# Kernel optimization log

Measured on AMD Instinct MI355X. Metric: run time of the kernel, lower is better.

## Reference

```python
import jax, jax.numpy as jnp
import numpy as np

N = 10000        # total_num
BS = 100         # batch_size (BatchNorm is applied per micro-batch in train mode)
IN_CH = 3
D = 128          # out_channels
TOPK = 50
BN_EPS = 1e-5


def setup_inputs() -> dict:
    key = jax.random.key(0)
    k1, k2, k3, k4 = jax.random.split(key, 4)
    feat = 32 * 32 * IN_CH
    inputs = jax.random.normal(k1, (N, IN_CH, 32, 32), dtype=jnp.float32)
    # nn.Linear(32*32*in_channels, out_channels)
    W1 = jax.random.normal(k2, (D, feat), dtype=jnp.float32) / np.sqrt(feat)
    b1 = jnp.zeros((D,), jnp.float32)
    # BatchNorm1d(out_channels) affine params
    gamma = jnp.ones((D,), jnp.float32)
    beta = jnp.zeros((D,), jnp.float32)
    # nn.Linear(out_channels, 1) -> weight [1, D] stored as vector, scalar bias
    sw = jax.random.normal(k3, (D,), dtype=jnp.float32) / np.sqrt(D)
    sb = jax.random.normal(k4, (), dtype=jnp.float32) * 0.01
    return {"inputs": inputs, "W1": W1, "b1": b1, "gamma": gamma,
            "beta": beta, "sw": sw, "sb": sb}


def _forward(inputs, W1, b1, gamma, beta, sw, sb):
    n = inputs.shape[0]
    # self.main is identity (undefined backbone); flatten + linear
    x = inputs.reshape(n, -1) @ W1.T + b1                      # [N, D]
    # BatchNorm1d in train mode, applied per batch of BS rows (as in the loop)
    xb = x.reshape(n // BS, BS, D)
    mean = xb.mean(axis=1, keepdims=True)
    var = xb.var(axis=1, keepdims=True)                        # biased, like torch BN
    outputs = ((xb - mean) * jax.lax.rsqrt(var + BN_EPS) * gamma + beta).reshape(n, D)
    # score[i,j] = ReLU( sum_k sw[k]*(x_i[k]-x_j[k])^2 + sb )
    a = (outputs * outputs) @ sw                               # [N]
    cross = (outputs * sw) @ outputs.T                         # [N, N]
    scores = jax.nn.relu(a[:, None] + a[None, :] - 2.0 * cross + sb)
    vals, idx = jax.lax.top_k(scores, TOPK)                    # [N, TOPK]
    vals = jax.nn.softmax(vals, axis=-1)
    S = jnp.zeros((n, n), outputs.dtype).at[jnp.arange(n)[:, None], idx].set(vals)
    return outputs, S


def reference(inputs, W1, b1, gamma, beta, sw, sb):
    return _forward(inputs, W1, b1, gamma, beta, sw, sb)
```

## Files before the change

### kernel.cpp

```cpp
#include <hip/hip_runtime.h>
#include <cstdint>

#define N_TOTAL 10000
#define D 128
#define FEAT 3072
#define BS_BN 100
#define TOPK 50

typedef unsigned int uint;
typedef short short8 __attribute__((ext_vector_type(8)));
typedef float f32x4 __attribute__((ext_vector_type(4)));
union U16 { uint4 u; short8 b; };

__device__ inline void split8(float4 f0, float4 f1, U16& h, U16& l) {
  float f[8] = {f0.x, f0.y, f0.z, f0.w, f1.x, f1.y, f1.z, f1.w};
  uint hb[8], lb[8];
#pragma unroll
  for (int e = 0; e < 8; ++e) {
    uint b = __float_as_uint(f[e]);
    uint hx = b & 0xFFFF0000u;
    float lf = f[e] - __uint_as_float(hx);
    hb[e] = b >> 16;
    lb[e] = __float_as_uint(lf) >> 16;
  }
  h.u = make_uint4(hb[0] | (hb[1] << 16), hb[2] | (hb[3] << 16),
                   hb[4] | (hb[5] << 16), hb[6] | (hb[7] << 16));
  l.u = make_uint4(lb[0] | (lb[1] << 16), lb[2] | (lb[3] << 16),
                   lb[4] | (lb[5] << 16), lb[6] | (lb[7] << 16));
}

__global__ __launch_bounds__(256) void k_gemm1(const float* __restrict__ in,
                                               const float* __restrict__ W1,
                                               float* __restrict__ x) {
  __shared__ float As[32][132];
  __shared__ float Bs[32][132];
  const int t = threadIdx.x;
  const int row0 = blockIdx.x * 128;
  const int k0 = blockIdx.y * 768;
  const int ty = t >> 4, tx = t & 15;
  const int i0 = ty * 8, j0 = tx * 8;
  float acc[8][8];
#pragma unroll
  for (int r = 0; r < 8; ++r)
#pragma unroll
    for (int c = 0; c < 8; ++c) acc[r][c] = 0.f;

  for (int kb = 0; kb < 768; kb += 32) {
    __syncthreads();
#pragma unroll
    for (int q = 0; q < 4; ++q) {
      int f = t + 256 * q;
      int row = f >> 3, kq = f & 7;
      int grow = row0 + row; if (grow >= N_TOTAL) grow = N_TOTAL - 1;
      float4 av = *(const float4*)(in + (size_t)grow * FEAT + k0 + kb + kq * 4);
      As[kq * 4 + 0][row] = av.x; As[kq * 4 + 1][row] = av.y;
      As[kq * 4 + 2][row] = av.z; As[kq * 4 + 3][row] = av.w;
      float4 bv = *(const float4*)(W1 + (size_t)row * FEAT + k0 + kb + kq * 4);
      Bs[kq * 4 + 0][row] = bv.x; Bs[kq * 4 + 1][row] = bv.y;
      Bs[kq * 4 + 2][row] = bv.z; Bs[kq * 4 + 3][row] = bv.w;
    }
    __syncthreads();
#pragma unroll
    for (int kk = 0; kk < 32; ++kk) {
      float4 a0 = *(const float4*)&As[kk][i0];
      float4 a1 = *(const float4*)&As[kk][i0 + 4];
      float4 b0 = *(const float4*)&Bs[kk][j0];
      float4 b1 = *(const float4*)&Bs[kk][j0 + 4];
      float av[8] = {a0.x, a0.y, a0.z, a0.w, a1.x, a1.y, a1.z, a1.w};
      float bv[8] = {b0.x, b0.y, b0.z, b0.w, b1.x, b1.y, b1.z, b1.w};
#pragma unroll
      for (int r = 0; r < 8; ++r)
#pragma unroll
        for (int c = 0; c < 8; ++c) acc[r][c] = fmaf(av[r], bv[c], acc[r][c]);
    }
  }
#pragma unroll
  for (int r = 0; r < 8; ++r) {
    int gi = row0 + i0 + r;
    if (gi < N_TOTAL) {
#pragma unroll
      for (int c = 0; c < 8; ++c)
        atomicAdd(&x[(size_t)gi * D + j0 + c], acc[r][c]);
    }
  }
}

__global__ __launch_bounds__(128) void k_bn(const float* __restrict__ x,
                                            const float* __restrict__ b1,
                                            const float* __restrict__ gamma,
                                            const float* __restrict__ beta,
                                            const float* __restrict__ sw,
                                            float* __restrict__ out_final,
                                            float* __restrict__ outf,
                                            float* __restrict__ wsw) {
  const int b = blockIdx.x, c = threadIdx.x;
  const float bias = b1[c];
  float s = 0.f, s2 = 0.f;
  const float* xp = x + (size_t)b * BS_BN * D + c;
  for (int r = 0; r < BS_BN; ++r) {
    float v = xp[(size_t)r * D] + bias;
    s += v; s2 = fmaf(v, v, s2);
  }
  float mean = s * (1.f / BS_BN);
  float var = s2 * (1.f / BS_BN) - mean * mean;
  float scale = gamma[c] * rsqrtf(var + 1e-5f);
  float shift = beta[c] - mean * scale;
  float swc = sw[c];
  float* op  = out_final + (size_t)b * BS_BN * D + c;
  float* ofp = outf + (size_t)b * BS_BN * D + c;
  float* wp  = wsw + (size_t)b * BS_BN * D + c;
  for (int r = 0; r < BS_BN; ++r) {
    float v = fmaf(xp[(size_t)r * D] + bias, scale, shift);
    op[(size_t)r * D] = v;
    ofp[(size_t)r * D] = v;
    wp[(size_t)r * D] = v * swc;
  }
}

__global__ __launch_bounds__(256) void k_arow(const float* __restrict__ outf,
                                              const float* __restrict__ sw,
                                              float* __restrict__ aarr) {
  const int t = threadIdx.x;
  const int lane = t & 63;
  const int row = blockIdx.x * 4 + (t >> 6);
  float o1 = outf[(size_t)row * D + lane];
  float o2 = outf[(size_t)row * D + 64 + lane];
  float v = sw[lane] * o1 * o1 + sw[64 + lane] * o2 * o2;
#pragma unroll
  for (int off = 32; off >= 1; off >>= 1) v += __shfl_xor(v, off);
  if (lane == 0) aarr[row] = v;
}

__global__ __launch_bounds__(256) void k_score(const float* __restrict__ outf,
                                               const float* __restrict__ wsw,
                                               const float* __restrict__ aarr,
                                               const float* __restrict__ sbp,
                                               float* __restrict__ S) {
  __shared__ alignas(16) float Af[128 * 44];
  __shared__ alignas(16) float Bf[128 * 44];
  const int t = threadIdx.x;
  const int lane = t & 63, wid = t >> 6;
  const int q = lane >> 4, l15 = lane & 15;
  const int ib = blockIdx.x * 128, jb = blockIdx.y * 128;
  const int wm = (wid & 1) * 64, wn = (wid >> 1) * 64;

  f32x4 acc[4][4];
#pragma unroll
  for (int mt = 0; mt < 4; ++mt)
#pragma unroll
    for (int nt = 0; nt < 4; ++nt) acc[mt][nt] = (f32x4){0.f, 0.f, 0.f, 0.f};

  for (int kb = 0; kb < D; kb += 32) {
    __syncthreads();
#pragma unroll
    for (int s = 0; s < 4; ++s) {
      int idx = t + 256 * s;
      int row = idx >> 3, f4 = (idx & 7) * 4;
      int gi = ib + row; if (gi > N_TOTAL - 1) gi = N_TOTAL - 1;
      int gj = jb + row; if (gj > N_TOTAL - 1) gj = N_TOTAL - 1;
      *(float4*)&Af[row * 44 + f4] = *(const float4*)&outf[(size_t)gi * D + kb + f4];
      *(float4*)&Bf[row * 44 + f4] = *(const float4*)&wsw[(size_t)gj * D + kb + f4];
    }
    __syncthreads();
    U16 Ah[4], Al[4], Bh[4], Bl[4];
#pragma unroll
    for (int mt = 0; mt < 4; ++mt) {
      int ro = (wm + mt * 16 + l15) * 44 + q * 8;
      float4 x0 = *(const float4*)&Af[ro];
      float4 x1 = *(const float4*)&Af[ro + 4];
      split8(x0, x1, Ah[mt], Al[mt]);
    }
#pragma unroll
    for (int nt = 0; nt < 4; ++nt) {
      int ro = (wn + nt * 16 + l15) * 44 + q * 8;
      float4 x0 = *(const float4*)&Bf[ro];
      float4 x1 = *(const float4*)&Bf[ro + 4];
      split8(x0, x1, Bh[nt], Bl[nt]);
    }
#pragma unroll
    for (int mt = 0; mt < 4; ++mt)
#pragma unroll
      for (int nt = 0; nt < 4; ++nt) {
        acc[mt][nt] = __builtin_amdgcn_mfma_f32_16x16x32_bf16(Ah[mt].b, Bh[nt].b, acc[mt][nt], 0, 0, 0);
        acc[mt][nt] = __builtin_amdgcn_mfma_f32_16x16x32_bf16(Ah[mt].b, Bl[nt].b, acc[mt][nt], 0, 0, 0);
        acc[mt][nt] = __builtin_amdgcn_mfma_f32_16x16x32_bf16(Al[mt].b, Bh[nt].b, acc[mt][nt], 0, 0, 0);
      }
  }

  const float sb = sbp[0];
  float ajv[4];
  int gjc[4];
#pragma unroll
  for (int nt = 0; nt < 4; ++nt) {
    gjc[nt] = jb + wn + nt * 16 + l15;
    ajv[nt] = aarr[gjc[nt] < N_TOTAL ? gjc[nt] : N_TOTAL - 1];
  }
#pragma unroll
  for (int mt = 0; mt < 4; ++mt) {
#pragma unroll
    for (int r = 0; r < 4; ++r) {
      int gi = ib + wm + mt * 16 + q * 4 + r;
      if (gi >= N_TOTAL) continue;
      float ai = aarr[gi] + sb;
#pragma unroll
      for (int nt = 0; nt < 4; ++nt) {
        if (gjc[nt] < N_TOTAL) {
          float s = ai + ajv[nt] - 2.f * acc[mt][nt][r];
          S[(size_t)gi * N_TOTAL + gjc[nt]] = (s > 0.f) ? s : 0.f;
        }
      }
    }
  }
}

__global__ __launch_bounds__(256) void k_topk(float* __restrict__ S) {
  const int t = threadIdx.x;
  const int lane = t & 63, wid = t >> 6;
  const size_t rbase = (size_t)blockIdx.x * N_TOTAL;
  const uint4* rp4v = (const uint4*)(S + rbase);

  uint v[10][4];
#pragma unroll
  for (int j = 0; j < 10; ++j) {
    if (j < 9 || t < 196) {
      uint4 x = rp4v[j * 256 + t];
      v[j][0] = x.x; v[j][1] = x.y; v[j][2] = x.z; v[j][3] = x.w;
    } else {
      v[j][0] = v[j][1] = v[j][2] = v[j][3] = 0u;
    }
  }

  __shared__ uint wred[4];
  __shared__ int scnt;
  __shared__ int ctr;
  __shared__ uint sT;
  __shared__ uint candv[1024];
  __shared__ float topv[TOPK];
  __shared__ int topi[TOPK];

  uint mx = 0u;
#pragma unroll
  for (int j = 0; j < 10; ++j)
#pragma unroll
    for (int e = 0; e < 4; ++e) mx = max(mx, v[j][e]);
#pragma unroll
  for (int off = 32; off >= 1; off >>= 1)
    mx = max(mx, (uint)__shfl_xor((int)mx, off));
  if (lane == 0) wred[wid] = mx;
  __syncthreads();
  mx = max(max(wred[0], wred[1]), max(wred[2], wred[3]));
  __syncthreads();

  uint T = 0u;
  bool zero_path = (mx == 0u);
  if (!zero_path) {
    uint C = mx & 0xFF800000u;
    if (C == 0u) C = 1u;
    uint Chi = mx + 1u;
    int cnt = 0, c_loc = 0;
    for (;;) {
      if (t == 0) scnt = 0;
      __syncthreads();
      c_loc = 0;
#pragma unroll
      for (int j = 0; j < 10; ++j)
#pragma unroll
        for (int e = 0; e < 4; ++e) c_loc += (v[j][e] >= C) ? 1 : 0;
      int cw = c_loc;
#pragma unroll
      for (int off = 32; off >= 1; off >>= 1) cw += __shfl_xor(cw, off);
      if (lane == 0) atomicAdd(&scnt, cw);
      __syncthreads();
      cnt = scnt;
      __syncthreads();
      if (cnt >= TOPK || C == 1u) break;
      Chi = C;
      C = (C > (1u << 23)) ? (C - (1u << 23)) : 1u;
    }
    if (cnt < TOPK) {
      zero_path = true;
    } else if (cnt <= 1024) {
      if (t == 0) ctr = 0;
      __syncthreads();
      int base_ = (c_loc > 0) ? atomicAdd(&ctr, c_loc) : 0;
      int p = base_;
#pragma unroll
      for (int j = 0; j < 10; ++j)
#pragma unroll
        for (int e = 0; e < 4; ++e)
          if (v[j][e] >= C) candv[p++] = v[j][e];
      __syncthreads();
      if (wid == 0) {
        uint cv[16];
#pragma unroll
        for (int s = 0; s < 16; ++s) {
          int ix = lane + s * 64;
          cv[s] = (ix < cnt) ? candv[ix] : 0u;
        }
        uint L = C, H = Chi;
        while (H - L > 1u) {
          uint M = L + ((H - L) >> 1);
          int cc = 0;
#pragma unroll
          for (int s = 0; s < 16; ++s) cc += (cv[s] >= M) ? 1 : 0;
#pragma unroll
          for (int off = 32; off >= 1; off >>= 1) cc += __shfl_xor(cc, off);
          if (cc >= TOPK) L = M; else H = M;
        }
        if (lane == 0) sT = L;
      }
      __syncthreads();
      T = sT;
    } else {
      uint L = C, H = Chi;
      while (H - L > 1u) {
        uint M = L + ((H - L) >> 1);
        if (t == 0) scnt = 0;
        __syncthreads();
        int c = 0;
#pragma unroll
        for (int j = 0; j < 10; ++j)
#pragma unroll
          for (int e = 0; e < 4; ++e) c += (v[j][e] >= M) ? 1 : 0;
#pragma unroll
        for (int off = 32; off >= 1; off >>= 1) c += __shfl_xor(c, off);
        if (lane == 0) atomicAdd(&scnt, c);
        __syncthreads();
        int f = scnt;
        __syncthreads();
        if (f >= TOPK) L = M; else H = M;
      }
      T = L;
    }
  }

  if (t == 0) ctr = 0;
  __syncthreads();
  int cg = 0;
#pragma unroll
  for (int j = 0; j < 10; ++j)
#pragma unroll
    for (int e = 0; e < 4; ++e) cg += (v[j][e] > T) ? 1 : 0;
  int gbase = (cg > 0) ? atomicAdd(&ctr, cg) : 0;
  {
    int p = gbase;
#pragma unroll
    for (int j = 0; j < 10; ++j)
#pragma unroll
      for (int e = 0; e < 4; ++e)
        if (v[j][e] > T) {
          if (p < TOPK) { topv[p] = __uint_as_float(v[j][e]); topi[p] = (j * 256 + t) * 4 + e; }
          ++p;
        }
  }
  __syncthreads();
  const int cnt_gt = min(ctr, TOPK);
  __syncthreads();
  const int need = TOPK - cnt_gt;

  if (!zero_path) {
    if (t == 0) scnt = 0;
    __syncthreads();
    int ce = 0;
#pragma unroll
    for (int j = 0; j < 10; ++j)
#pragma unroll
      for (int e = 0; e < 4; ++e) ce += (v[j][e] == T) ? 1 : 0;
    int ebase = (ce > 0) ? atomicAdd(&scnt, ce) : 0;
    {
      int p = ebase;
#pragma unroll
      for (int j = 0; j < 10; ++j)
#pragma unroll
        for (int e = 0; e < 4; ++e)
          if (v[j][e] == T) {
            if (p < 1024) candv[p] = (uint)((j * 256 + t) * 4 + e);
            ++p;
          }
    }
    __syncthreads();
    int nE = min(scnt, 1024);
    if (wid == 0) {
      int es[16];
#pragma unroll
      for (int s = 0; s < 16; ++s) {
        int ix = lane + s * 64;
        es[s] = (ix < nE) ? (int)candv[ix] : 0x7FFFFFFF;
      }
      for (int r = 0; r < need; ++r) {
        int m = es[0];
#pragma unroll
        for (int s = 1; s < 16; ++s) m = min(m, es[s]);
#pragma unroll
        for (int off = 32; off >= 1; off >>= 1) m = min(m, __shfl_xor(m, off));
        if (lane == 0 && m != 0x7FFFFFFF) {
          topv[cnt_gt + r] = __uint_as_float(T);
          topi[cnt_gt + r] = m;
        }
#pragma unroll
        for (int s = 0; s < 16; ++s) if (es[s] == m) es[s] = 0x7FFFFFFF;
      }
    }
    __syncthreads();
  } else {
    int L = 0, H = N_TOTAL;
    while (H - L > 1) {
      int M = L + ((H - L) >> 1);
      if (t == 0) scnt = 0;
      __syncthreads();
      int c = 0;
#pragma unroll
      for (int j = 0; j < 10; ++j)
#pragma unroll
        for (int e = 0; e < 4; ++e) {
          int col = (j * 256 + t) * 4 + e;
          c += (v[j][e] == 0u && col < M) ? 1 : 0;
        }
#pragma unroll
      for (int off = 32; off >= 1; off >>= 1) c += __shfl_xor(c, off);
      if (lane == 0) atomicAdd(&scnt, c);
      __syncthreads();
      int f = scnt;
      __syncthreads();
      if (f >= need) H = M; else L = M;
    }
    if (t == 0) scnt = 0;
    __syncthreads();
    int cz = 0;
#pragma unroll
    for (int j = 0; j < 10; ++j)
#pragma unroll
      for (int e = 0; e < 4; ++e) {
        int col = (j * 256 + t) * 4 + e;
        cz += (v[j][e] == 0u && col < H) ? 1 : 0;
      }
    int zbase = (cz > 0) ? atomicAdd(&scnt, cz) : 0;
    {
      int p = zbase;
#pragma unroll
      for (int j = 0; j < 10; ++j)
#pragma unroll
        for (int e = 0; e < 4; ++e) {
          int col = (j * 256 + t) * 4 + e;
          if (v[j][e] == 0u && col < H) {
            if (cnt_gt + p < TOPK) { topv[cnt_gt + p] = 0.0f; topi[cnt_gt + p] = col; }
            ++p;
          }
        }
    }
    __syncthreads();
  }

  if (wid == 0) {
    float xv = (lane < TOPK) ? topv[lane] : -1e30f;
    float mxf = xv;
#pragma unroll
    for (int off = 32; off >= 1; off >>= 1) mxf = fmaxf(mxf, __shfl_xor(mxf, off));
    float e = (lane < TOPK) ? expf(xv - mxf) : 0.f;
    float ss = e;
#pragma unroll
    for (int off = 32; off >= 1; off >>= 1) ss += __shfl_xor(ss, off);
    if (lane < TOPK) topv[lane] = e / ss;
  }
  __syncthreads();

  float4 z = make_float4(0.f, 0.f, 0.f, 0.f);
  float4* wp4 = (float4*)(S + rbase);
  for (int i = t; i < N_TOTAL / 4; i += 256) wp4[i] = z;
  __syncthreads();
  if (t < TOPK) {
    int ii = topi[t];
    if (ii >= 0 && ii < N_TOTAL) S[rbase + ii] = topv[t];
  }
}

extern "C" void kernel_launch(void* const* d_in, const int* in_sizes, int n_in,
                              void* d_out, int out_size, void* d_ws, size_t ws_size,
                              hipStream_t stream) {
  const float* in    = (const float*)d_in[0];
  const float* W1    = (const float*)d_in[1];
  const float* b1    = (const float*)d_in[2];
  const float* gamma = (const float*)d_in[3];
  const float* beta  = (const float*)d_in[4];
  const float* sw    = (const float*)d_in[5];
  const float* sb    = (const float*)d_in[6];
  float* out_f = (float*)d_out;
  float* S = out_f + (size_t)N_TOTAL * D;

  float* wsf  = (float*)d_ws;
  float* x    = wsf;
  float* outf = wsf + 1280000;
  float* wswb = wsf + 2560000;
  float* aarr = wsf + 3840000;

  hipMemsetAsync(x, 0, (size_t)N_TOTAL * D * sizeof(float), stream);
  k_gemm1<<<dim3(79, 4), 256, 0, stream>>>(in, W1, x);
  k_bn<<<100, 128, 0, stream>>>(x, b1, gamma, beta, sw, out_f, outf, wswb);
  k_arow<<<2500, 256, 0, stream>>>(outf, sw, aarr);
  k_score<<<dim3(79, 79), 256, 0, stream>>>(outf, wswb, aarr, sb, S);
  k_topk<<<10000, 256, 0, stream>>>(S);
}
```

Measured before the change: 1.030 ms.

## Use split-bf16 MFMA for the input projection GEMM

```diff
diff --git a/kernel.cpp b/kernel.cpp
--- a/kernel.cpp
+++ b/kernel.cpp
@@ -32,55 +32,66 @@
 __global__ __launch_bounds__(256) void k_gemm1(const float* __restrict__ in,
                                                const float* __restrict__ W1,
                                                float* __restrict__ x) {
-  __shared__ float As[32][132];
-  __shared__ float Bs[32][132];
+  __shared__ alignas(16) float Af[128 * 44];
+  __shared__ alignas(16) float Bf[128 * 44];
   const int t = threadIdx.x;
-  const int row0 = blockIdx.x * 128;
+  const int lane = t & 63, wid = t >> 6;
+  const int q = lane >> 4, l15 = lane & 15;
+  const int i0 = blockIdx.x * 128;
   const int k0 = blockIdx.y * 768;
-  const int ty = t >> 4, tx = t & 15;
-  const int i0 = ty * 8, j0 = tx * 8;
-  float acc[8][8];
-#pragma unroll
-  for (int r = 0; r < 8; ++r)
-#pragma unroll
-    for (int c = 0; c < 8; ++c) acc[r][c] = 0.f;
-
-  for (int kb = 0; kb < 768; kb += 32) {
-    __syncthreads();
-#pragma unroll
-    for (int q = 0; q < 4; ++q) {
-      int f = t + 256 * q;
-      int row = f >> 3, kq = f & 7;
-      int grow = row0 + row; if (grow >= N_TOTAL) grow = N_TOTAL - 1;
-      float4 av = *(const float4*)(in + (size_t)grow * FEAT + k0 + kb + kq * 4);
-      As[kq * 4 + 0][row] = av.x; As[kq * 4 + 1][row] = av.y;
-      As[kq * 4 + 2][row] = av.z; As[kq * 4 + 3][row] = av.w;
-      float4 bv = *(const float4*)(W1 + (size_t)row * FEAT + k0 + kb + kq * 4);
-      Bs[kq * 4 + 0][row] = bv.x; Bs[kq * 4 + 1][row] = bv.y;
-      Bs[kq * 4 + 2][row] = bv.z; Bs[kq * 4 + 3][row] = bv.w;
-    }
-    __syncthreads();
-#pragma unroll
-    for (int kk = 0; kk < 32; ++kk) {
-      float4 a0 = *(const float4*)&As[kk][i0];
-      float4 a1 = *(const float4*)&As[kk][i0 + 4];
-      float4 b0 = *(const float4*)&Bs[kk][j0];
-      float4 b1 = *(const float4*)&Bs[kk][j0 + 4];
-      float av[8] = {a0.x, a0.y, a0.z, a0.w, a1.x, a1.y, a1.z, a1.w};
-      float bv[8] = {b0.x, b0.y, b0.z, b0.w, b1.x, b1.y, b1.z, b1.w};
-#pragma unroll
-      for (int r = 0; r < 8; ++r)
-#pragma unroll
-        for (int c = 0; c < 8; ++c) acc[r][c] = fmaf(av[r], bv[c], acc[r][c]);
-    }
-  }
-#pragma unroll
-  for (int r = 0; r < 8; ++r) {
-    int gi = row0 + i0 + r;
-    if (gi < N_TOTAL) {
-#pragma unroll
-      for (int c = 0; c < 8; ++c)
-        atomicAdd(&x[(size_t)gi * D + j0 + c], acc[r][c]);
+  const int wm = (wid & 1) * 64, wn = (wid >> 1) * 64;
+
+  f32x4 acc[4][4];
+#pragma unroll
+  for (int mt = 0; mt < 4; ++mt)
+#pragma unroll
+    for (int nt = 0; nt < 4; ++nt) acc[mt][nt] = (f32x4){0.f, 0.f, 0.f, 0.f};
+
+  for (int kb = k0; kb < k0 + 768; kb += 32) {
+    __syncthreads();
+#pragma unroll
+    for (int s = 0; s < 4; ++s) {
+      int idx = t + 256 * s;
+      int row = idx >> 3, f4 = (idx & 7) * 4;
+      int gi = i0 + row; if (gi > N_TOTAL - 1) gi = N_TOTAL - 1;
+      *(float4*)&Af[row * 44 + f4] = *(const float4*)&in[(size_t)gi * FEAT + kb + f4];
+      *(float4*)&Bf[row * 44 + f4] = *(const float4*)&W1[(size_t)row * FEAT + kb + f4];
+    }
+    __syncthreads();
+    U16 Ah[4], Al[4], Bh[4], Bl[4];
+#pragma unroll
+    for (int mt = 0; mt < 4; ++mt) {
+      int ro = (wm + mt * 16 + l15) * 44 + q * 8;
+      float4 x0 = *(const float4*)&Af[ro];
+      float4 x1 = *(const float4*)&Af[ro + 4];
+      split8(x0, x1, Ah[mt], Al[mt]);
+    }
+#pragma unroll
+    for (int nt = 0; nt < 4; ++nt) {
+      int ro = (wn + nt * 16 + l15) * 44 + q * 8;
+      float4 x0 = *(const float4*)&Bf[ro];
+      float4 x1 = *(const float4*)&Bf[ro + 4];
+      split8(x0, x1, Bh[nt], Bl[nt]);
+    }
+#pragma unroll
+    for (int mt = 0; mt < 4; ++mt)
+#pragma unroll
+      for (int nt = 0; nt < 4; ++nt) {
+        acc[mt][nt] = __builtin_amdgcn_mfma_f32_16x16x32_bf16(Ah[mt].b, Bh[nt].b, acc[mt][nt], 0, 0, 0);
+        acc[mt][nt] = __builtin_amdgcn_mfma_f32_16x16x32_bf16(Ah[mt].b, Bl[nt].b, acc[mt][nt], 0, 0, 0);
+        acc[mt][nt] = __builtin_amdgcn_mfma_f32_16x16x32_bf16(Al[mt].b, Bh[nt].b, acc[mt][nt], 0, 0, 0);
+      }
+  }
+
+#pragma unroll
+  for (int mt = 0; mt < 4; ++mt) {
+#pragma unroll
+    for (int r = 0; r < 4; ++r) {
+      int gi = i0 + wm + mt * 16 + q * 4 + r;
+      if (gi >= N_TOTAL) continue;
+#pragma unroll
+      for (int nt = 0; nt < 4; ++nt)
+        atomicAdd(&x[(size_t)gi * D + wn + nt * 16 + l15], acc[mt][nt][r]);
     }
   }
 }
```

New measurement: 905.2 us. 1.14x faster.
